# Kernel tuning notes

Hardware: AMD Instinct MI355X
Metric: run time of the kernel (lower is better)

Reference implementation:

```python
import jax, jax.numpy as jnp
import numpy as np

STATE_LEN = 4096
SEQ_LEN = 8192
T = 1024  # number of time buckets in time_sim_mat


def setup_inputs() -> dict:
    key = jax.random.key(0)
    k1, k2, k3 = jax.random.split(key, 3)
    his = jax.random.randint(k1, (SEQ_LEN,), 0, T, dtype=jnp.int64 if jax.config.jax_enable_x64 else jnp.int32)
    cur = jax.random.randint(k2, (STATE_LEN,), 0, T, dtype=jnp.int64 if jax.config.jax_enable_x64 else jnp.int32)
    time_sim_mat = jax.random.normal(k3, (T, T), dtype=jnp.float32)
    return {"his": his, "cur": cur, "time_sim_mat": time_sim_mat}


def reference(his, cur, time_sim_mat):
    # attn_energies[i, j] = time_sim_mat[cur[i], his[j]]  (vectorized gather)
    energies = time_sim_mat[cur[:, None], his[None, :]]  # [state_len, seq_len]
    return jax.nn.softmax(energies, axis=-1)
```

## Files before the change

### kernel.cpp

```cpp
#include <hip/hip_runtime.h>
#include <cstddef>

#define TDIM 1024
#define SEQ 8192
#define NROWS 4096

__global__ __launch_bounds__(256) void hist_kernel(const int* __restrict__ his,
                                                   int* __restrict__ counts) {
    __shared__ int lc[TDIM];
    const int tid = threadIdx.x;
    for (int t = tid; t < TDIM; t += 256) lc[t] = 0;
    __syncthreads();
    const int base = blockIdx.x * 1024;
    for (int i = tid; i < 1024; i += 256) {
        int h = his[base + i];
        atomicAdd(&lc[h], 1);
    }
    __syncthreads();
    for (int t = tid; t < TDIM; t += 256) {
        int c = lc[t];
        if (c) atomicAdd(&counts[t], c);
    }
}

__global__ __launch_bounds__(256) void softmax_gather_kernel(
    const int* __restrict__ his, const int* __restrict__ cur,
    const float* __restrict__ M, const int* __restrict__ counts,
    float* __restrict__ out)
{
    __shared__ float prob[TDIM];
    __shared__ float red[16];
    const int tid = threadIdx.x;
    const int row = blockIdx.x;
    const int r = cur[row];
    const float* Mrow = M + (size_t)r * TDIM;

    float m[4];
    int   c[4];
#pragma unroll
    for (int k = 0; k < 4; ++k) {
        int t = tid + 256 * k;
        m[k] = Mrow[t];
        c[k] = counts[t];
    }

    float lmax = -3.402823466e38f;
#pragma unroll
    for (int k = 0; k < 4; ++k)
        if (c[k] > 0) lmax = fmaxf(lmax, m[k]);
#pragma unroll
    for (int off = 32; off > 0; off >>= 1)
        lmax = fmaxf(lmax, __shfl_down(lmax, off, 64));
    const int wave = tid >> 6, lane = tid & 63;
    if (lane == 0) red[wave] = lmax;
    __syncthreads();
    if (tid == 0) {
        float g = red[0];
        for (int w = 1; w < 4; ++w) g = fmaxf(g, red[w]);
        red[8] = g;
    }
    __syncthreads();
    const float gmax = red[8];

    float e[4];
    float lsum = 0.f;
#pragma unroll
    for (int k = 0; k < 4; ++k) {
        e[k] = __expf(m[k] - gmax);
        lsum += (float)c[k] * e[k];
    }
#pragma unroll
    for (int off = 32; off > 0; off >>= 1)
        lsum += __shfl_down(lsum, off, 64);
    if (lane == 0) red[4 + wave] = lsum;
    __syncthreads();
    if (tid == 0) {
        float s = red[4] + red[5] + red[6] + red[7];
        red[9] = 1.0f / s;
    }
    __syncthreads();
    const float inv = red[9];

#pragma unroll
    for (int k = 0; k < 4; ++k)
        prob[tid + 256 * k] = e[k] * inv;
    __syncthreads();

    const int4* his4 = (const int4*)his;
    float4* out4 = (float4*)(out + (size_t)row * SEQ);
#pragma unroll
    for (int it = 0; it < 8; ++it) {
        int j4 = it * 256 + tid;
        int4 h = his4[j4];
        float4 o;
        o.x = prob[h.x];
        o.y = prob[h.y];
        o.z = prob[h.z];
        o.w = prob[h.w];
        out4[j4] = o;
    }
}

extern "C" void kernel_launch(void* const* d_in, const int* in_sizes, int n_in,
                              void* d_out, int out_size, void* d_ws, size_t ws_size,
                              hipStream_t stream) {
    const int*   his = (const int*)d_in[0];
    const int*   cur = (const int*)d_in[1];
    const float* M   = (const float*)d_in[2];
    float* out = (float*)d_out;
    int* counts = (int*)d_ws;

    hipMemsetAsync(counts, 0, TDIM * sizeof(int), stream);
    hist_kernel<<<8, 256, 0, stream>>>(his, counts);
    softmax_gather_kernel<<<NROWS, 256, 0, stream>>>(his, cur, M, counts, out);
}
```

Before: 148.2 us.

## Precompute softmax rows per unique time bucket and replicate them by cur

Adds a kernel that computes the softmax-gathered row once for each of the 1024 possible cur values into a workspace buffer. A second kernel then copies the matching precomputed row into each of the 4096 output rows, using nontemporal vector stores. The aim is to cut the redundant per-row reduction and LDS gather work by about four times and turn the main pass into a streaming copy. In exchange it adds a 32 MB intermediate write and read. The new path only runs when the workspace is large enough; otherwise it falls back to the old kernel.

```diff
diff --git a/kernel.cpp b/kernel.cpp
--- a/kernel.cpp
+++ b/kernel.cpp
@@ -4,6 +4,8 @@
 #define TDIM 1024
 #define SEQ 8192
 #define NROWS 4096
+
+typedef float f32x4 __attribute__((ext_vector_type(4)));
 
 __global__ __launch_bounds__(256) void hist_kernel(const int* __restrict__ his,
                                                    int* __restrict__ counts) {
@@ -20,6 +22,98 @@
     for (int t = tid; t < TDIM; t += 256) {
         int c = lc[t];
         if (c) atomicAdd(&counts[t], c);
+    }
+}
+
+__global__ __launch_bounds__(256) void unique_row_kernel(
+    const int* __restrict__ his, const float* __restrict__ M,
+    const int* __restrict__ counts, float* __restrict__ G)
+{
+    __shared__ float prob[TDIM];
+    __shared__ float red[16];
+    const int tid = threadIdx.x;
+    const int r = blockIdx.x;
+    const float* Mrow = M + (size_t)r * TDIM;
+
+    float m[4];
+    int   c[4];
+#pragma unroll
+    for (int k = 0; k < 4; ++k) {
+        int t = tid + 256 * k;
+        m[k] = Mrow[t];
+        c[k] = counts[t];
+    }
+
+    float lmax = -3.402823466e38f;
+#pragma unroll
+    for (int k = 0; k < 4; ++k)
+        if (c[k] > 0) lmax = fmaxf(lmax, m[k]);
+#pragma unroll
+    for (int off = 32; off > 0; off >>= 1)
+        lmax = fmaxf(lmax, __shfl_down(lmax, off, 64));
+    const int wave = tid >> 6, lane = tid & 63;
+    if (lane == 0) red[wave] = lmax;
+    __syncthreads();
+    if (tid == 0) {
+        float g = red[0];
+        for (int w = 1; w < 4; ++w) g = fmaxf(g, red[w]);
+        red[8] = g;
+    }
+    __syncthreads();
+    const float gmax = red[8];
+
+    float e[4];
+    float lsum = 0.f;
+#pragma unroll
+    for (int k = 0; k < 4; ++k) {
+        e[k] = __expf(m[k] - gmax);
+        lsum += (float)c[k] * e[k];
+    }
+#pragma unroll
+    for (int off = 32; off > 0; off >>= 1)
+        lsum += __shfl_down(lsum, off, 64);
+    if (lane == 0) red[4 + wave] = lsum;
+    __syncthreads();
+    if (tid == 0) {
+        float s = red[4] + red[5] + red[6] + red[7];
+        red[9] = 1.0f / s;
+    }
+    __syncthreads();
+    const float inv = red[9];
+
+#pragma unroll
+    for (int k = 0; k < 4; ++k)
+        prob[tid + 256 * k] = e[k] * inv;
+    __syncthreads();
+
+    const int4* his4 = (const int4*)his;
+    f32x4* g4 = (f32x4*)(G + (size_t)r * SEQ);
+#pragma unroll
+    for (int it = 0; it < 8; ++it) {
+        int j4 = it * 256 + tid;
+        int4 h = his4[j4];
+        f32x4 o;
+        o.x = prob[h.x];
+        o.y = prob[h.y];
+        o.z = prob[h.z];
+        o.w = prob[h.w];
+        g4[j4] = o;
+    }
+}
+
+__global__ __launch_bounds__(256) void replicate_kernel(
+    const int* __restrict__ cur, const float* __restrict__ G,
+    float* __restrict__ out)
+{
+    const int row = blockIdx.x;
+    const int r = cur[row];
+    const f32x4* __restrict__ src = (const f32x4*)(G + (size_t)r * SEQ);
+    f32x4* __restrict__ dst = (f32x4*)(out + (size_t)row * SEQ);
+#pragma unroll
+    for (int it = 0; it < 8; ++it) {
+        int j = it * 256 + threadIdx.x;
+        f32x4 v = src[j];
+        __builtin_nontemporal_store(v, &dst[j]);
     }
 }
 
@@ -110,7 +204,16 @@
     float* out = (float*)d_out;
     int* counts = (int*)d_ws;
 
+    const size_t need = 4096 + (size_t)TDIM * SEQ * sizeof(float);
+
     hipMemsetAsync(counts, 0, TDIM * sizeof(int), stream);
     hist_kernel<<<8, 256, 0, stream>>>(his, counts);
-    softmax_gather_kernel<<<NROWS, 256, 0, stream>>>(his, cur, M, counts, out);
-}
+
+    if (ws_size >= need) {
+        float* G = (float*)((char*)d_ws + 4096);
+        unique_row_kernel<<<TDIM, 256, 0, stream>>>(his, M, counts, G);
+        replicate_kernel<<<NROWS, 256, 0, stream>>>(cur, G, out);
+    } else {
+        softmax_gather_kernel<<<NROWS, 256, 0, stream>>>(his, cur, M, counts, out);
+    }
+}
```

After: 173.3 us. 16.9% more time.

## Fuse histogram into softmax-gather kernel, recomputing counts per block

Applied to the files above, without the earlier changes.

Drops the memset and the separate histogram kernel. Each of the 4096 blocks now rebuilds the 8192-entry histogram of his in shared memory with LDS atomics, keeping his in registers for the final gather. It also removes two barriers by having every thread combine the per-wave reductions itself. This saves two launches and the global atomics. In exchange, every block redoes 8192 LDS atomics and keeps 32 more registers live.

```diff
diff --git a/kernel.cpp b/kernel.cpp
--- a/kernel.cpp
+++ b/kernel.cpp
@@ -5,44 +5,47 @@
 #define SEQ 8192
 #define NROWS 4096
 
-__global__ __launch_bounds__(256) void hist_kernel(const int* __restrict__ his,
-                                                   int* __restrict__ counts) {
+typedef float f32x4 __attribute__((ext_vector_type(4)));
+
+__global__ __launch_bounds__(256) void fused_kernel(
+    const int* __restrict__ his, const int* __restrict__ cur,
+    const float* __restrict__ M, float* __restrict__ out)
+{
     __shared__ int lc[TDIM];
-    const int tid = threadIdx.x;
-    for (int t = tid; t < TDIM; t += 256) lc[t] = 0;
-    __syncthreads();
-    const int base = blockIdx.x * 1024;
-    for (int i = tid; i < 1024; i += 256) {
-        int h = his[base + i];
-        atomicAdd(&lc[h], 1);
-    }
-    __syncthreads();
-    for (int t = tid; t < TDIM; t += 256) {
-        int c = lc[t];
-        if (c) atomicAdd(&counts[t], c);
-    }
-}
+    __shared__ float red[8];
+    float* prob = (float*)lc;
 
-__global__ __launch_bounds__(256) void softmax_gather_kernel(
-    const int* __restrict__ his, const int* __restrict__ cur,
-    const float* __restrict__ M, const int* __restrict__ counts,
-    float* __restrict__ out)
-{
-    __shared__ float prob[TDIM];
-    __shared__ float red[16];
     const int tid = threadIdx.x;
     const int row = blockIdx.x;
     const int r = cur[row];
     const float* Mrow = M + (size_t)r * TDIM;
 
+#pragma unroll
+    for (int k = 0; k < 4; ++k) lc[tid + 256 * k] = 0;
+
+    const int4* his4 = (const int4*)his;
+    int4 h[8];
+#pragma unroll
+    for (int it = 0; it < 8; ++it) h[it] = his4[it * 256 + tid];
+
     float m[4];
-    int   c[4];
 #pragma unroll
-    for (int k = 0; k < 4; ++k) {
-        int t = tid + 256 * k;
-        m[k] = Mrow[t];
-        c[k] = counts[t];
+    for (int k = 0; k < 4; ++k) m[k] = Mrow[tid + 256 * k];
+
+    __syncthreads();
+
+#pragma unroll
+    for (int it = 0; it < 8; ++it) {
+        atomicAdd(&lc[h[it].x], 1);
+        atomicAdd(&lc[h[it].y], 1);
+        atomicAdd(&lc[h[it].z], 1);
+        atomicAdd(&lc[h[it].w], 1);
     }
+    __syncthreads();
+
+    int c[4];
+#pragma unroll
+    for (int k = 0; k < 4; ++k) c[k] = lc[tid + 256 * k];
 
     float lmax = -3.402823466e38f;
 #pragma unroll
@@ -54,13 +57,7 @@
     const int wave = tid >> 6, lane = tid & 63;
     if (lane == 0) red[wave] = lmax;
     __syncthreads();
-    if (tid == 0) {
-        float g = red[0];
-        for (int w = 1; w < 4; ++w) g = fmaxf(g, red[w]);
-        red[8] = g;
-    }
-    __syncthreads();
-    const float gmax = red[8];
+    const float gmax = fmaxf(fmaxf(red[0], red[1]), fmaxf(red[2], red[3]));
 
     float e[4];
     float lsum = 0.f;
@@ -74,30 +71,22 @@
         lsum += __shfl_down(lsum, off, 64);
     if (lane == 0) red[4 + wave] = lsum;
     __syncthreads();
-    if (tid == 0) {
-        float s = red[4] + red[5] + red[6] + red[7];
-        red[9] = 1.0f / s;
-    }
-    __syncthreads();
-    const float inv = red[9];
+    const float inv = 1.0f / (red[4] + red[5] + red[6] + red[7]);
 
 #pragma unroll
     for (int k = 0; k < 4; ++k)
         prob[tid + 256 * k] = e[k] * inv;
     __syncthreads();
 
-    const int4* his4 = (const int4*)his;
-    float4* out4 = (float4*)(out + (size_t)row * SEQ);
+    f32x4* out4 = (f32x4*)(out + (size_t)row * SEQ);
 #pragma unroll
     for (int it = 0; it < 8; ++it) {
-        int j4 = it * 256 + tid;
-        int4 h = his4[j4];
-        float4 o;
-        o.x = prob[h.x];
-        o.y = prob[h.y];
-        o.z = prob[h.z];
-        o.w = prob[h.w];
-        out4[j4] = o;
+        f32x4 o;
+        o.x = prob[h[it].x];
+        o.y = prob[h[it].y];
+        o.z = prob[h[it].z];
+        o.w = prob[h[it].w];
+        out4[it * 256 + tid] = o;
     }
 }
 
@@ -108,9 +97,7 @@
     const int*   cur = (const int*)d_in[1];
     const float* M   = (const float*)d_in[2];
     float* out = (float*)d_out;
-    int* counts = (int*)d_ws;
+    (void)d_ws; (void)ws_size;
 
-    hipMemsetAsync(counts, 0, TDIM * sizeof(int), stream);
-    hist_kernel<<<8, 256, 0, stream>>>(his, counts);
-    softmax_gather_kernel<<<NROWS, 256, 0, stream>>>(his, cur, M, counts, out);
+    fused_kernel<<<NROWS, 256, 0, stream>>>(his, cur, M, out);
 }
```

Result: faster. 143.6 us (-3.1%).
